# Kernel optimization log

Hardware: AMD Instinct MI355X
Metric: run time of the kernel (lower is better)

Reference implementation:

```python
import jax, jax.numpy as jnp
import numpy as np

N_PTS0 = 32   # samples per line
N_PTS1 = 8    # after maxpool (scale factor 4)
DIM_LOI = 128
DIM_FC = 1024
FEAT_DIM = 8
HW = 128      # feature-map spatial size (hardcoded via clamp(max=127) in source)


def setup_inputs() -> dict:
    key = jax.random.key(0)
    ks = jax.random.split(key, 11)
    B, L = 8, 5000
    feature = jax.random.normal(ks[0], (B, 256, HW, HW), jnp.float32)
    # line endpoints in pixel coords [0, 128)
    p = jax.random.uniform(ks[1], (B, L, 2, 2), jnp.float32) * HW
    feat = jax.random.normal(ks[2], (B, L, FEAT_DIM), jnp.float32)
    W_fc1 = jax.random.normal(ks[3], (DIM_LOI, 256), jnp.float32) * 0.05
    b_fc1 = jnp.zeros((DIM_LOI,), jnp.float32)
    d_in = DIM_LOI * N_PTS1 + FEAT_DIM  # 1032
    W1 = jax.random.normal(ks[4], (d_in, DIM_FC), jnp.float32) * 0.03
    b1 = jnp.zeros((DIM_FC,), jnp.float32)
    W2 = jax.random.normal(ks[5], (DIM_FC, DIM_FC), jnp.float32) * 0.03
    b2 = jnp.zeros((DIM_FC,), jnp.float32)
    W3 = jax.random.normal(ks[6], (DIM_FC, 1), jnp.float32) * 0.03
    b3 = jnp.zeros((1,), jnp.float32)
    return dict(feature=feature, p=p, feat=feat, W_fc1=W_fc1, b_fc1=b_fc1,
                W1=W1, b1=b1, W2=W2, b2=b2, W3=W3, b3=b3)


def _loi_head(feature, p, feat, W_fc1, b_fc1, W1, b1, W2, b2, W3, b3):
    B, _, H, W = feature.shape
    L = p.shape[1]
    # fc1: 1x1 conv -> [B, DIM_LOI, H, W]
    x = jnp.einsum('bchw,dc->bdhw', feature, W_fc1) + b_fc1[None, :, None, None]

    # sample N_PTS0 points along each line: [B, L, 32, 2]
    lam = jnp.linspace(0.0, 1.0, N_PTS0, dtype=p.dtype)[:, None]
    pts = p[:, :, 0:1, :] * lam + p[:, :, 1:2, :] * (1.0 - lam) - 0.5
    px, py = pts[..., 0], pts[..., 1]
    px0 = jnp.clip(jnp.floor(px), 0.0, HW - 1)
    py0 = jnp.clip(jnp.floor(py), 0.0, HW - 1)
    px1 = jnp.clip(px0 + 1.0, 0.0, HW - 1)
    py1 = jnp.clip(py0 + 1.0, 0.0, HW - 1)
    px0i, py0i = px0.astype(jnp.int32), py0.astype(jnp.int32)
    px1i, py1i = px1.astype(jnp.int32), py1.astype(jnp.int32)

    # bilinear blend weights [B, L, 32] -> broadcast over channel dim
    w00 = ((px1 - px) * (py1 - py))[:, None]
    w10 = ((px - px0) * (py1 - py))[:, None]
    w01 = ((px1 - px) * (py - py0))[:, None]
    w11 = ((px - px0) * (py - py0))[:, None]

    gather = jax.vmap(lambda xb, ix, iy: xb[:, ix, iy])  # [C,L,32] per image
    xp = (gather(x, px0i, py0i) * w00 + gather(x, px1i, py0i) * w10 +
          gather(x, px0i, py1i) * w01 + gather(x, px1i, py1i) * w11)  # [B,C,L,32]
    xp = jnp.transpose(xp, (0, 2, 1, 3))  # [B, L, C, 32]

    # MaxPool1d(kernel=4, stride=4) over sampled points -> [B, L, C, 8]
    pooled = xp.reshape(B, L, DIM_LOI, N_PTS1, N_PTS0 // N_PTS1).max(-1)
    flat = pooled.reshape(B, L, DIM_LOI * N_PTS1)
    z = jnp.concatenate([flat, feat], axis=-1)  # [B, L, 1032]

    h = jax.nn.relu(z @ W1 + b1)
    h = jax.nn.relu(h @ W2 + b2)
    logits = (h @ W3 + b3)[..., 0]  # [B, L]
    return logits


def reference(feature, p, feat, W_fc1, b_fc1, W1, b1, W2, b2, W3, b3):
    return _loi_head(feature, p, feat, W_fc1, b_fc1, W1, b1, W2, b2, W3, b3)
```

## Files before the change

kernel.cpp:

```cpp
#include <hip/hip_runtime.h>

typedef _Float16 f16;
typedef __fp16 h16x2 __attribute__((ext_vector_type(2)));
typedef f16 f16x8 __attribute__((ext_vector_type(8)));
typedef float f32x4 __attribute__((ext_vector_type(4)));

#define HW    128
#define NPIX  16384
#define CDIM  256
#define DLOI  128
#define LROWS 40000
#define DFC   1024
#define KP1   1088

__global__ __launch_bounds__(256, 4) void conv1x1_kernel(
    const float* __restrict__ feature, const float* __restrict__ Wfc,
    const float* __restrict__ bfc, f16* __restrict__ x) {
  const int tid = threadIdx.x;
  const int l = tid & 63;
  const int w = tid >> 6;
  const int bid = blockIdx.x;
  const int b = bid & 7;
  const int pix0 = (bid >> 3) * 128;
  const int wr = (w >> 1) * 64;
  const int wc = (w & 1) * 64;
  const int lrow = l & 15;
  const int g4 = l >> 4;

  const float* fb = feature + (size_t)b * CDIM * NPIX;
  f32x4 acc[4][4] = {};

  auto loadA = [&](int kb, int m, float* av) {
    const int pix = pix0 + wr + m * 16 + lrow;
    const float* ap = fb + (size_t)kb * NPIX + pix;
#pragma unroll
    for (int j = 0; j < 8; ++j) av[j] = ap[(size_t)j * NPIX];
  };

  float avA[8], avB[8];
  loadA(g4 * 8, 0, avA);

#pragma unroll
  for (int kf = 0; kf < 8; ++kf) {
    const int kb = kf * 32 + g4 * 8;
    f16x8 bf[4];
#pragma unroll
    for (int n = 0; n < 4; ++n) {
      const float* wp = &Wfc[(size_t)(wc + n * 16 + lrow) * CDIM + kb];
      float4 w0 = *(const float4*)wp;
      float4 w1 = *(const float4*)(wp + 4);
      union { f16x8 v; h16x2 h[4]; } u;
      u.h[0] = __builtin_amdgcn_cvt_pkrtz(w0.x, w0.y);
      u.h[1] = __builtin_amdgcn_cvt_pkrtz(w0.z, w0.w);
      u.h[2] = __builtin_amdgcn_cvt_pkrtz(w1.x, w1.y);
      u.h[3] = __builtin_amdgcn_cvt_pkrtz(w1.z, w1.w);
      bf[n] = u.v;
    }
#pragma unroll
    for (int m = 0; m < 4; ++m) {
      float* cur = (m & 1) ? avB : avA;
      float* nxt = (m & 1) ? avA : avB;
      if (m < 3)       loadA(kb, m + 1, nxt);
      else if (kf < 7) loadA(kb + 32, 0, nxt);
      union { f16x8 v; h16x2 h[4]; } u;
      u.h[0] = __builtin_amdgcn_cvt_pkrtz(cur[0], cur[1]);
      u.h[1] = __builtin_amdgcn_cvt_pkrtz(cur[2], cur[3]);
      u.h[2] = __builtin_amdgcn_cvt_pkrtz(cur[4], cur[5]);
      u.h[3] = __builtin_amdgcn_cvt_pkrtz(cur[6], cur[7]);
#pragma unroll
      for (int n = 0; n < 4; ++n)
        acc[m][n] = __builtin_amdgcn_mfma_f32_16x16x32_f16(u.v, bf[n], acc[m][n], 0, 0, 0);
    }
  }

#pragma unroll
  for (int m = 0; m < 4; ++m) {
#pragma unroll
    for (int r = 0; r < 4; ++r) {
      const int pix = pix0 + wr + m * 16 + g4 * 4 + r;
      f16* xr = x + ((size_t)b * NPIX + pix) * DLOI;
#pragma unroll
      for (int n = 0; n < 4; ++n) {
        const int d = wc + n * 16 + lrow;
        xr[d] = (f16)(acc[m][n][r] + bfc[d]);
      }
    }
  }
}

__global__ __launch_bounds__(256) void sample_kernel(
    const f16* __restrict__ x, const float* __restrict__ p,
    const float* __restrict__ feat, f16* __restrict__ z) {
  const int tid = threadIdx.x;
  const int wv = tid >> 6;
  const int lane = tid & 63;
  const int sub = lane >> 4;
  const int cl = lane & 15;
  const int bid = blockIdx.x;
  const int b = bid & 7;
  const int row = b * 5000 + (bid >> 3) * 4 + wv;

  const float4 pe = *(const float4*)&p[(size_t)row * 4];
  const size_t bb = (size_t)b * NPIX;
  f16* zr = z + (size_t)row * KP1;

#pragma unroll
  for (int gh = 0; gh < 2; ++gh) {
    const int g = gh * 4 + sub;
    float acc[8];
#pragma unroll
    for (int ci = 0; ci < 8; ++ci) acc[ci] = -1e30f;
#pragma unroll
    for (int pt = 0; pt < 4; ++pt) {
      const int t = g * 4 + pt;
      const float lam = (float)t * (1.0f / 31.0f);
      const float px = pe.x * lam + pe.z * (1.f - lam) - 0.5f;
      const float py = pe.y * lam + pe.w * (1.f - lam) - 0.5f;
      const float px0 = fminf(fmaxf(floorf(px), 0.f), 127.f);
      const float py0 = fminf(fmaxf(floorf(py), 0.f), 127.f);
      const float px1 = fminf(px0 + 1.f, 127.f);
      const float py1 = fminf(py0 + 1.f, 127.f);
      const int ix0 = (int)px0, iy0 = (int)py0, ix1 = (int)px1, iy1 = (int)py1;
      const float w00 = (px1 - px) * (py1 - py);
      const float w10 = (px - px0) * (py1 - py);
      const float w01 = (px1 - px) * (py - py0);
      const float w11 = (px - px0) * (py - py0);

      const f16* r00 = x + (bb + ix0 * HW + iy0) * DLOI + cl * 8;
      const f16* r10 = x + (bb + ix1 * HW + iy0) * DLOI + cl * 8;
      const f16* r01 = x + (bb + ix0 * HW + iy1) * DLOI + cl * 8;
      const f16* r11 = x + (bb + ix1 * HW + iy1) * DLOI + cl * 8;
      f16x8 a  = *(const f16x8*)r00;
      f16x8 bq = *(const f16x8*)r10;
      f16x8 cq = *(const f16x8*)r01;
      f16x8 dq = *(const f16x8*)r11;
#pragma unroll
      for (int ci = 0; ci < 8; ++ci) {
        float m = w00 * (float)a[ci] + w10 * (float)bq[ci] +
                  w01 * (float)cq[ci] + w11 * (float)dq[ci];
        acc[ci] = fmaxf(acc[ci], m);
      }
    }
    f16x8 o;
#pragma unroll
    for (int ci = 0; ci < 8; ++ci) o[ci] = (f16)acc[ci];
    *(f16x8*)(zr + g * 128 + cl * 8) = o;
  }
  if (lane < 8) zr[1024 + lane] = (f16)feat[(size_t)row * 8 + lane];
  else if (lane < 36) *(unsigned int*)((char*)zr + 2064 + (lane - 8) * 4) = 0u;
}

__global__ __launch_bounds__(256) void wtrans_kernel(
    const float* __restrict__ W, f16* __restrict__ Wt, int K, int ldt, int permute) {
  __shared__ float t[32][33];
  const int tx = threadIdx.x & 31, ty = threadIdx.x >> 5;
#pragma unroll
  for (int i = 0; i < 4; ++i) {
    int kd = blockIdx.y * 32 + ty + i * 8;
    int ks = (permute && kd < 1024) ? ((kd & 127) * 8 + (kd >> 7)) : kd;
    int n = blockIdx.x * 32 + tx;
    t[ty + i * 8][tx] = (ks < K) ? W[(size_t)ks * DFC + n] : 0.f;
  }
  __syncthreads();
#pragma unroll
  for (int i = 0; i < 4; ++i) {
    int n = blockIdx.x * 32 + ty + i * 8;
    int k = blockIdx.y * 32 + tx;
    Wt[(size_t)n * ldt + k] = (f16)t[tx][ty + i * 8];
  }
}

#define GEMM_MAIN_LOOP(A_, Bt_, M_, ksteps_, lda_)                              \
  __shared__ f16 As[256 * 64];                                                  \
  __shared__ f16 Bs[128 * 64];                                                  \
  const int tid = threadIdx.x;                                                  \
  const int l = tid & 63;                                                       \
  const int w = tid >> 6;                                                       \
  const int nwg = gridDim.x;                                  \
  const int s = (blockIdx.x & 7) * (nwg >> 3) + (blockIdx.x >> 3);              \
  const int m0 = (s >> 3) * 256;                                                \
  const int n0 = (s & 7) * 128;                                                 \
  const int wr = (w >> 1) * 64, wc = (w & 1) * 64;                              \
  const int srow = tid >> 3;                                         \
  const int slot = tid & 7;                                                     \
  const int lrow = l & 15, g4 = l >> 4;                                         \
  f32x4 acc[4][4] = {};                                                         \
  for (int kt = 0; kt < ksteps_; ++kt) {                                        \
    const int kb = kt * 64;                                                     \
    __syncthreads();                                                            \
    _Pragma("unroll")                                                           \
    for (int c = 0; c < 4; ++c) {                                               \
      int row = c * 64 + srow;                                                  \
      int arow = m0 + row; if (arow >= M_) arow = M_ - 1;                       \
      const f16* g = A_ + (size_t)arow * lda_ + kb + ((slot ^ (row & 7)) * 8);  \
      __builtin_amdgcn_global_load_lds(                                         \
          (const __attribute__((address_space(1))) void*)g,                     \
          (__attribute__((address_space(3))) void*)(As + row * 64 + slot * 8),  \
          16, 0, 0);                                                            \
    }                                                                           \
    _Pragma("unroll")                                                           \
    for (int c = 0; c < 2; ++c) {                                               \
      int row = c * 64 + srow;                                                  \
      const f16* g = Bt_ + (size_t)(n0 + row) * lda_ + kb + ((slot ^ (row & 7)) * 8); \
      __builtin_amdgcn_global_load_lds(                                         \
          (const __attribute__((address_space(1))) void*)g,                     \
          (__attribute__((address_space(3))) void*)(Bs + row * 64 + slot * 8),  \
          16, 0, 0);                                                            \
    }                                                                           \
    __syncthreads();                                                            \
    _Pragma("unroll")                                                           \
    for (int kh = 0; kh < 2; ++kh) {                                            \
      f16x8 af[4], bf[4];                                                       \
      _Pragma("unroll")                                                         \
      for (int m = 0; m < 4; ++m) {                                             \
        int row = wr + m * 16 + lrow;                                           \
        int sl = (g4 + 4 * kh) ^ (row & 7);                                     \
        af[m] = *(const f16x8*)(As + row * 64 + sl * 8);                        \
      }                                                                         \
      _Pragma("unroll")                                                         \
      for (int n = 0; n < 4; ++n) {                                             \
        int row = wc + n * 16 + lrow;                                           \
        int sl = (g4 + 4 * kh) ^ (row & 7);                                     \
        bf[n] = *(const f16x8*)(Bs + row * 64 + sl * 8);                        \
      }                                                                         \
      _Pragma("unroll")                                                         \
      for (int m = 0; m < 4; ++m)                                               \
        _Pragma("unroll")                                                       \
        for (int n = 0; n < 4; ++n)                                             \
          acc[m][n] = __builtin_amdgcn_mfma_f32_16x16x32_f16(af[m], bf[n], acc[m][n], 0, 0, 0); \
    }                                                                           \
  }

__global__ __launch_bounds__(512, 4) void gemm_f16(
    const f16* __restrict__ A, const f16* __restrict__ Bt,
    const float* __restrict__ bias, f16* __restrict__ C,
    int M, int ksteps, int lda) {
  GEMM_MAIN_LOOP(A, Bt, M, ksteps, lda)

  const int ocol0 = n0 + wc + lrow;
  const int orow0 = m0 + wr + g4 * 4;
#pragma unroll
  for (int m = 0; m < 4; ++m) {
#pragma unroll
    for (int r = 0; r < 4; ++r) {
      int orow = orow0 + m * 16 + r;
      if (orow >= M) continue;
      f16* crow = C + (size_t)orow * DFC;
#pragma unroll
      for (int n = 0; n < 4; ++n) {
        int col = ocol0 + n * 16;
        float v = acc[m][n][r] + bias[col];
        crow[col] = (f16)fmaxf(v, 0.f);
      }
    }
  }
}

__global__ __launch_bounds__(512, 4) void gemm2_fc3(
    const f16* __restrict__ A, const f16* __restrict__ Bt,
    const float* __restrict__ bias, const float* __restrict__ W3,
    float* __restrict__ out, int M, int ksteps, int lda) {
  GEMM_MAIN_LOOP(A, Bt, M, ksteps, lda)

  const int ocol0 = n0 + wc + lrow;
  const int orow0 = m0 + wr + g4 * 4;
  float b4[4], w3v[4];
#pragma unroll
  for (int n = 0; n < 4; ++n) {
    b4[n] = bias[ocol0 + n * 16];
    w3v[n] = W3[ocol0 + n * 16];
  }
#pragma unroll
  for (int m = 0; m < 4; ++m) {
#pragma unroll
    for (int r = 0; r < 4; ++r) {
      float sacc = 0.f;
#pragma unroll
      for (int n = 0; n < 4; ++n) {
        float v = fmaxf(acc[m][n][r] + b4[n], 0.f);
        sacc += v * w3v[n];
      }
      sacc += __shfl_xor(sacc, 1);
      sacc += __shfl_xor(sacc, 2);
      sacc += __shfl_xor(sacc, 4);
      sacc += __shfl_xor(sacc, 8);
      int orow = orow0 + m * 16 + r;
      if (lrow == 0 && orow < M) atomicAdd(&out[orow], sacc);
    }
  }
}

__global__ __launch_bounds__(256) void fill_out(
    float* __restrict__ out, const float* __restrict__ b3, int n) {
  int i = blockIdx.x * 256 + threadIdx.x;
  if (i < n) out[i] = b3[0];
}

extern "C" void kernel_launch(void* const* d_in, const int* in_sizes, int n_in,
                              void* d_out, int out_size, void* d_ws, size_t ws_size,
                              hipStream_t stream) {
  const float* feature = (const float*)d_in[0];
  const float* p       = (const float*)d_in[1];
  const float* feat    = (const float*)d_in[2];
  const float* W_fc1   = (const float*)d_in[3];
  const float* b_fc1   = (const float*)d_in[4];
  const float* W1      = (const float*)d_in[5];
  const float* b1      = (const float*)d_in[6];
  const float* W2      = (const float*)d_in[7];
  const float* b2      = (const float*)d_in[8];
  const float* W3      = (const float*)d_in[9];
  const float* b3      = (const float*)d_in[10];
  float* out = (float*)d_out;

  char* ws = (char*)d_ws;
  f16* x   = (f16*)(ws + 0);
  f16* z   = (f16*)(ws + 33554432ULL);
  f16* h1  = (f16*)(ws + 120594432ULL);
  f16* W1t = (f16*)(ws + 202514432ULL);
  f16* W2t = (f16*)(ws + 204742656ULL);

  hipLaunchKernelGGL(wtrans_kernel, dim3(32, 34), dim3(256), 0, stream,
                     W1, W1t, 1032, KP1, 1);
  hipLaunchKernelGGL(wtrans_kernel, dim3(32, 32), dim3(256), 0, stream,
                     W2, W2t, 1024, 1024, 0);
  hipLaunchKernelGGL(conv1x1_kernel, dim3(1024), dim3(256), 0, stream,
                     feature, W_fc1, b_fc1, x);
  hipLaunchKernelGGL(sample_kernel, dim3(10000), dim3(256), 0, stream,
                     x, p, feat, z);
  hipLaunchKernelGGL(gemm_f16, dim3(1256), dim3(512), 0, stream,
                     z, W1t, b1, h1, LROWS, KP1 / 64, KP1);
  hipLaunchKernelGGL(fill_out, dim3(157), dim3(256), 0, stream,
                     out, b3, LROWS);
  hipLaunchKernelGGL(gemm2_fc3, dim3(1256), dim3(512), 0, stream,
                     h1, W2t, b2, W3, out, LROWS, DFC / 64, DFC);
}
```

Measured before the change: 332.6 us.

## Triple-buffer GEMM LDS tiles with async global-to-LDS prefetch two steps ahead

The shared GEMM main loop now keeps three LDS buffers for the A and B tiles and issues global_load_lds for step k+2 while computing step k. A partial vmcnt wait replaces the previous full sync around each load. The goal is to hide global memory latency behind MFMA work. LDS use triples to 144KB per block, so launch bounds drop to 2 blocks per CU, which lowers occupancy. The explicit vmcnt(12) count must match the number of outstanding loads.

```diff
diff --git a/kernel.cpp b/kernel.cpp
--- a/kernel.cpp
+++ b/kernel.cpp
@@ -171,8 +171,8 @@
 }
 
 #define GEMM_MAIN_LOOP(A_, Bt_, M_, ksteps_, lda_)                              \
-  __shared__ f16 As[256 * 64];                                                  \
-  __shared__ f16 Bs[128 * 64];                                                  \
+  __shared__ f16 As[3][256 * 64];                                               \
+  __shared__ f16 Bs[3][128 * 64];                                               \
   const int tid = threadIdx.x;                                                  \
   const int l = tid & 63;                                                       \
   const int w = tid >> 6;                                                       \
@@ -185,9 +185,7 @@
   const int slot = tid & 7;                                                     \
   const int lrow = l & 15, g4 = l >> 4;                                         \
   f32x4 acc[4][4] = {};                                                         \
-  for (int kt = 0; kt < ksteps_; ++kt) {                                        \
-    const int kb = kt * 64;                                                     \
-    __syncthreads();                                                            \
+  auto stage = [&](f16* Ad, f16* Bd, int kb) {                                  \
     _Pragma("unroll")                                                           \
     for (int c = 0; c < 4; ++c) {                                               \
       int row = c * 64 + srow;                                                  \
@@ -195,7 +193,7 @@
       const f16* g = A_ + (size_t)arow * lda_ + kb + ((slot ^ (row & 7)) * 8);  \
       __builtin_amdgcn_global_load_lds(                                         \
           (const __attribute__((address_space(1))) void*)g,                     \
-          (__attribute__((address_space(3))) void*)(As + row * 64 + slot * 8),  \
+          (__attribute__((address_space(3))) void*)(Ad + row * 64 + slot * 8),  \
           16, 0, 0);                                                            \
     }                                                                           \
     _Pragma("unroll")                                                           \
@@ -204,10 +202,22 @@
       const f16* g = Bt_ + (size_t)(n0 + row) * lda_ + kb + ((slot ^ (row & 7)) * 8); \
       __builtin_amdgcn_global_load_lds(                                         \
           (const __attribute__((address_space(1))) void*)g,                     \
-          (__attribute__((address_space(3))) void*)(Bs + row * 64 + slot * 8),  \
+          (__attribute__((address_space(3))) void*)(Bd + row * 64 + slot * 8),  \
           16, 0, 0);                                                            \
     }                                                                           \
-    __syncthreads();                                                            \
+  };                                                                            \
+  f16 *a0 = &As[0][0], *a1 = &As[1][0], *a2 = &As[2][0];                        \
+  f16 *b0 = &Bs[0][0], *b1 = &Bs[1][0], *b2 = &Bs[2][0];                        \
+  stage(a0, b0, 0);                                                             \
+  stage(a1, b1, 64);                               \
+  for (int kt = 0; kt < ksteps_; ++kt) {                                        \
+    const int kb2 = (kt + 2 < ksteps_ ? kt + 2 : ksteps_ - 1) * 64;             \
+    stage(a2, b2, kb2);                    \
+    asm volatile("s_waitcnt vmcnt(12)" ::: "memory");  \
+    __builtin_amdgcn_s_barrier();                                               \
+    __builtin_amdgcn_sched_barrier(0);                                          \
+    const f16* AsB = a0;                                                        \
+    const f16* BsB = b0;                                                        \
     _Pragma("unroll")                                                           \
     for (int kh = 0; kh < 2; ++kh) {                                            \
       f16x8 af[4], bf[4];                                                       \
@@ -215,13 +225,13 @@
       for (int m = 0; m < 4; ++m) {                                             \
         int row = wr + m * 16 + lrow;                                           \
         int sl = (g4 + 4 * kh) ^ (row & 7);                                     \
-        af[m] = *(const f16x8*)(As + row * 64 + sl * 8);                        \
+        af[m] = *(const f16x8*)(AsB + row * 64 + sl * 8);                       \
       }                                                                         \
       _Pragma("unroll")                                                         \
       for (int n = 0; n < 4; ++n) {                                             \
         int row = wc + n * 16 + lrow;                                           \
         int sl = (g4 + 4 * kh) ^ (row & 7);                                     \
-        bf[n] = *(const f16x8*)(Bs + row * 64 + sl * 8);                        \
+        bf[n] = *(const f16x8*)(BsB + row * 64 + sl * 8);                       \
       }                                                                         \
       _Pragma("unroll")                                                         \
       for (int m = 0; m < 4; ++m)                                               \
@@ -229,9 +239,14 @@
         for (int n = 0; n < 4; ++n)                                             \
           acc[m][n] = __builtin_amdgcn_mfma_f32_16x16x32_f16(af[m], bf[n], acc[m][n], 0, 0, 0); \
     }                                                                           \
-  }
-
-__global__ __launch_bounds__(512, 4) void gemm_f16(
+    __builtin_amdgcn_sched_barrier(0);                                          \
+    __builtin_amdgcn_s_barrier();         \
+    __builtin_amdgcn_sched_barrier(0);                                          \
+    f16* ta = a0; a0 = a1; a1 = a2; a2 = ta;                                    \
+    f16* tb = b0; b0 = b1; b1 = b2; b2 = tb;                                    \
+  }
+
+__global__ __launch_bounds__(512, 2) void gemm_f16(
     const f16* __restrict__ A, const f16* __restrict__ Bt,
     const float* __restrict__ bias, f16* __restrict__ C,
     int M, int ksteps, int lda) {
@@ -256,7 +271,7 @@
   }
 }
 
-__global__ __launch_bounds__(512, 4) void gemm2_fc3(
+__global__ __launch_bounds__(512, 2) void gemm2_fc3(
     const f16* __restrict__ A, const f16* __restrict__ Bt,
     const float* __restrict__ bias, const float* __restrict__ W3,
     float* __restrict__ out, int M, int ksteps, int lda) {
```

Measured after the change: 403.5 us. +21.3%, slower.

## Stage conv1x1 operand tiles in LDS via direct global-to-LDS loads with swizzle

Applied to the files above, without the earlier changes.

The 1x1 conv GEMM now copies 32-channel K-slices of the feature map and weights into shared memory using global_load_lds, with XOR-swizzled layouts, and then reads MFMA fragments from LDS. Before, each lane did strided scalar global loads straight into registers with software double buffering. The goal is coalesced global traffic and less register pressure. In exchange there are two block barriers per K-tile, no overlap between loading and compute, and 32KB of LDS per block, which may limit occupancy.

```diff
diff --git a/kernel.cpp b/kernel.cpp
--- a/kernel.cpp
+++ b/kernel.cpp
@@ -16,57 +16,84 @@
 __global__ __launch_bounds__(256, 4) void conv1x1_kernel(
     const float* __restrict__ feature, const float* __restrict__ Wfc,
     const float* __restrict__ bfc, f16* __restrict__ x) {
+  __shared__ float As[32 * 128];
+  __shared__ float Bs[128 * 32];
   const int tid = threadIdx.x;
   const int l = tid & 63;
   const int w = tid >> 6;
   const int bid = blockIdx.x;
   const int b = bid & 7;
   const int pix0 = (bid >> 3) * 128;
-  const int wr = (w >> 1) * 64;
-  const int wc = (w & 1) * 64;
-  const int lrow = l & 15;
-  const int g4 = l >> 4;
+  const int wr = (w >> 1) * 64, wc = (w & 1) * 64;
+  const int lrow = l & 15, g4 = l >> 4;
 
   const float* fb = feature + (size_t)b * CDIM * NPIX;
   f32x4 acc[4][4] = {};
 
-  auto loadA = [&](int kb, int m, float* av) {
-    const int pix = pix0 + wr + m * 16 + lrow;
-    const float* ap = fb + (size_t)kb * NPIX + pix;
-#pragma unroll
-    for (int j = 0; j < 8; ++j) av[j] = ap[(size_t)j * NPIX];
-  };
-
-  float avA[8], avB[8];
-  loadA(g4 * 8, 0, avA);
-
-#pragma unroll
-  for (int kf = 0; kf < 8; ++kf) {
-    const int kb = kf * 32 + g4 * 8;
+  const int a_cslot = tid & 31;
+  const int a_pixl  = tid >> 5;
+  const int a_c     = a_cslot ^ (a_pixl << 2);
+  const int b_dl    = tid >> 3;
+  const int b_coff  = ((tid & 7) ^ (b_dl & 7)) * 4;
+
+  const int aX = (lrow & 7) << 2;
+  const int s1 = (g4 * 8) ^ aX;
+  const int s2 = (g4 * 8 + 4) ^ aX;
+
+  for (int kt = 0; kt < 8; ++kt) {
+    const int kb = kt * 32;
+    __syncthreads();
+    {
+      const float* g = fb + (size_t)(kb + a_c) * NPIX + pix0 + a_pixl;
+      float* d = As + a_pixl * 32 + a_cslot;
+#pragma unroll
+      for (int pass = 0; pass < 16; ++pass) {
+        __builtin_amdgcn_global_load_lds(
+            (const __attribute__((address_space(1))) void*)g,
+            (__attribute__((address_space(3))) void*)d, 4, 0, 0);
+        g += 8;
+        d += 256;
+      }
+    }
+    {
+      const float* g = Wfc + (size_t)b_dl * CDIM + kb + b_coff;
+      float* d = Bs + b_dl * 32 + (tid & 7) * 4;
+#pragma unroll
+      for (int pass = 0; pass < 4; ++pass) {
+        __builtin_amdgcn_global_load_lds(
+            (const __attribute__((address_space(1))) void*)g,
+            (__attribute__((address_space(3))) void*)d, 16, 0, 0);
+        g += (size_t)32 * CDIM;
+        d += 32 * 32;
+      }
+    }
+    __syncthreads();
+
     f16x8 bf[4];
 #pragma unroll
     for (int n = 0; n < 4; ++n) {
-      const float* wp = &Wfc[(size_t)(wc + n * 16 + lrow) * CDIM + kb];
-      float4 w0 = *(const float4*)wp;
-      float4 w1 = *(const float4*)(wp + 4);
+      const int d = wc + n * 16 + lrow;
+      const int c1 = (2 * g4) ^ (d & 7);
+      const int c2 = (2 * g4 + 1) ^ (d & 7);
+      f32x4 lo = *(const f32x4*)(Bs + d * 32 + c1 * 4);
+      f32x4 hi = *(const f32x4*)(Bs + d * 32 + c2 * 4);
       union { f16x8 v; h16x2 h[4]; } u;
-      u.h[0] = __builtin_amdgcn_cvt_pkrtz(w0.x, w0.y);
-      u.h[1] = __builtin_amdgcn_cvt_pkrtz(w0.z, w0.w);
-      u.h[2] = __builtin_amdgcn_cvt_pkrtz(w1.x, w1.y);
-      u.h[3] = __builtin_amdgcn_cvt_pkrtz(w1.z, w1.w);
+      u.h[0] = __builtin_amdgcn_cvt_pkrtz(lo[0], lo[1]);
+      u.h[1] = __builtin_amdgcn_cvt_pkrtz(lo[2], lo[3]);
+      u.h[2] = __builtin_amdgcn_cvt_pkrtz(hi[0], hi[1]);
+      u.h[3] = __builtin_amdgcn_cvt_pkrtz(hi[2], hi[3]);
       bf[n] = u.v;
     }
 #pragma unroll
     for (int m = 0; m < 4; ++m) {
-      float* cur = (m & 1) ? avB : avA;
-      float* nxt = (m & 1) ? avA : avB;
-      if (m < 3)       loadA(kb, m + 1, nxt);
-      else if (kf < 7) loadA(kb + 32, 0, nxt);
+      const int pix = wr + m * 16 + lrow;
+      f32x4 lo = *(const f32x4*)(As + pix * 32 + s1);
+      f32x4 hi = *(const f32x4*)(As + pix * 32 + s2);
       union { f16x8 v; h16x2 h[4]; } u;
-      u.h[0] = __builtin_amdgcn_cvt_pkrtz(cur[0], cur[1]);
-      u.h[1] = __builtin_amdgcn_cvt_pkrtz(cur[2], cur[3]);
-      u.h[2] = __builtin_amdgcn_cvt_pkrtz(cur[4], cur[5]);
-      u.h[3] = __builtin_amdgcn_cvt_pkrtz(cur[6], cur[7]);
+      u.h[0] = __builtin_amdgcn_cvt_pkrtz(lo[0], lo[1]);
+      u.h[1] = __builtin_amdgcn_cvt_pkrtz(lo[2], lo[3]);
+      u.h[2] = __builtin_amdgcn_cvt_pkrtz(hi[0], hi[1]);
+      u.h[3] = __builtin_amdgcn_cvt_pkrtz(hi[2], hi[3]);
 #pragma unroll
       for (int n = 0; n < 4; ++n)
         acc[m][n] = __builtin_amdgcn_mfma_f32_16x16x32_f16(u.v, bf[n], acc[m][n], 0, 0, 0);
```

Measured after the change: 341.7 us. 1.03x slower.
